# Performance work log

Hardware: AMD Instinct MI355X
Metric: run time of the kernel (lower is better)

The kernel has to match this reference:

```python
import jax, jax.numpy as jnp
import numpy as np

B, IN, H, F, T = 4096, 1024, 1024, 128, 3
LN_EPS = 1e-5


def setup_inputs() -> dict:
    key = jax.random.key(0)
    ks = jax.random.split(key, 12)
    inp = {
        "input_": jax.random.normal(ks[0], (B, IN), jnp.float32),
        "hx": jax.random.normal(ks[1], (B, H), jnp.float32),
        "cx": jax.random.normal(ks[2], (B, H), jnp.float32),
        "topic_w": jax.random.uniform(ks[3], (B, T), jnp.float32),
        # factorized gate weights (init scales per reset_parameters)
        "w_ih_a": jax.random.normal(ks[4], (4 * H, F), jnp.float32) / jnp.sqrt(F),
        "w_ih_b": jnp.full((F, T), 0.1 / T, jnp.float32),
        "w_ih_c": jax.random.normal(ks[5], (F, IN), jnp.float32) / jnp.sqrt(IN),
        "w_hh_a": 0.1 * jax.random.normal(ks[6], (4 * H, F), jnp.float32),
        "w_hh_b": jnp.full((F, T), 0.1 / T, jnp.float32),
        "w_hh_c": 0.1 * jax.random.normal(ks[7], (F, H), jnp.float32),
        # theta transforms: weight=0, bias=1 per reset_parameters
        "th_ih_w": jnp.zeros((T, T), jnp.float32),
        "th_ih_b": jnp.ones((T,), jnp.float32),
        "th_hh_w": jnp.zeros((T, T), jnp.float32),
        "th_hh_b": jnp.ones((T,), jnp.float32),
        # layernorm params
        "ln_i_w": jnp.ones((4 * H,), jnp.float32),
        "ln_i_b": jnp.zeros((4 * H,), jnp.float32),
        "ln_h_w": jnp.ones((4 * H,), jnp.float32),
        "ln_h_b": jnp.zeros((4 * H,), jnp.float32),
        "ln_c_w": jnp.ones((H,), jnp.float32),
        "ln_c_b": jnp.zeros((H,), jnp.float32),
    }
    return inp


def _ln(x, w, b):
    mu = x.mean(-1, keepdims=True)
    var = ((x - mu) ** 2).mean(-1, keepdims=True)
    return (x - mu) * jax.lax.rsqrt(var + LN_EPS) * w + b


def reference(input_, hx, cx, topic_w,
              w_ih_a, w_ih_b, w_ih_c, w_hh_a, w_hh_b, w_hh_c,
              th_ih_w, th_ih_b, th_hh_w, th_hh_b,
              ln_i_w, ln_i_b, ln_h_w, ln_h_b, ln_c_w, ln_c_b):
    # factorized input gates: ((x @ C^T) * (theta(topic) @ B^T)) @ A^T
    scale_i = (topic_w @ th_ih_w.T + th_ih_b) @ w_ih_b.T            # [B, F]
    igates = ((input_ @ w_ih_c.T) * scale_i) @ w_ih_a.T             # [B, 4H]
    scale_h = (topic_w @ th_hh_w.T + th_hh_b) @ w_hh_b.T            # [B, F]
    hgates = ((hx @ w_hh_c.T) * scale_h) @ w_hh_a.T                 # [B, 4H]

    gates = _ln(igates, ln_i_w, ln_i_b) + _ln(hgates, ln_h_w, ln_h_b)
    i, f, g, o = jnp.split(gates, 4, axis=1)
    i = jax.nn.sigmoid(i)
    f = jax.nn.sigmoid(f)
    g = jnp.tanh(g)  # dropout p=0 -> identity
    o = jax.nn.sigmoid(o)
    cy = _ln(f * cx + i * g, ln_c_w, ln_c_b)
    hy = o * jnp.tanh(cy)
    return hy, cy
```

## Files before the change

kernel.cpp:

```cpp
#include <hip/hip_runtime.h>

typedef unsigned short ushort_t;
typedef __attribute__((ext_vector_type(8))) short bf8_t;
typedef __attribute__((ext_vector_type(4))) float f4_t;

#define B_   4096
#define IN_  1024
#define H_   1024
#define F_   128
#define EPS_ 1e-5f

#define NG1   1024
#define NPREP 256
#define NGRAM 128

__device__ __forceinline__ float us2f(unsigned short s) {
  union { unsigned int u; float f; } v;
  v.u = ((unsigned int)s) << 16;
  return v.f;
}
__device__ __forceinline__ unsigned short f2us(float f) {
  union { float f; unsigned int u; } v;
  v.f = f;
  unsigned int r = (v.u + 0x7fffu + ((v.u >> 16) & 1u)) >> 16;
  return (unsigned short)r;
}
__device__ __forceinline__ float sigf(float x) { return 1.0f / (1.0f + __expf(-x)); }
__device__ __forceinline__ float tanh_f(float x) { return 1.0f - 2.0f / (1.0f + __expf(2.0f * x)); }

__device__ __forceinline__ int detect_fp32(const void* disc) {
  return ((const unsigned int*)disc)[0] == 0x3F800000u;
}
__device__ __forceinline__ float ldf(const void* p, int i, int fp32) {
  return fp32 ? ((const float*)p)[i] : us2f(((const ushort_t*)p)[i]);
}
__device__ __forceinline__ void ld8(const void* p, int idx, float* o, int fp32) {
  if (fp32) {
    const float4* q = (const float4*)((const float*)p + idx);
    float4 v0 = q[0], v1 = q[1];
    o[0]=v0.x; o[1]=v0.y; o[2]=v0.z; o[3]=v0.w;
    o[4]=v1.x; o[5]=v1.y; o[6]=v1.z; o[7]=v1.w;
  } else {
    uint4 v = *(const uint4*)((const ushort_t*)p + idx);
    const ushort_t* pv = (const ushort_t*)&v;
    #pragma unroll
    for (int i = 0; i < 8; i++) o[i] = us2f(pv[i]);
  }
}
__device__ __forceinline__ bf8_t cvt8p(const float* f) {
  union { bf8_t v; unsigned int u[4]; } r;
  const unsigned int* ui = (const unsigned int*)f;
  #pragma unroll
  for (int i = 0; i < 4; i++) {
    unsigned int lo = ui[2 * i] + 0x8000u;
    unsigned int hi = ui[2 * i + 1] + 0x8000u;
    r.u[i] = __builtin_amdgcn_perm(hi, lo, 0x07060302u);
  }
  return r.v;
}

__global__ __launch_bounds__(256, 8) void k_stageA(
    const void* __restrict__ X0, const void* __restrict__ X1,
    const void* __restrict__ Wc0, const void* __restrict__ Wc1,
    const void* __restrict__ Ai, const void* __restrict__ Ah,
    const void* __restrict__ lnwi, const void* __restrict__ lnwh,
    ushort_t* __restrict__ wb,
    float* __restrict__ cm_i, float* __restrict__ cm_h,
    float* __restrict__ g_i, float* __restrict__ g_h,
    float* __restrict__ C0, float* __restrict__ C1)
{
  __shared__ __align__(16) char lds_raw[16384];
  int bid = blockIdx.x, tid = threadIdx.x;
  int fp32 = detect_fp32(lnwi);

  if (bid < NG1) {
    int rb = bid >> 2, mat = (bid >> 1) & 1, kh = bid & 1;
    const void* X = mat ? X1 : X0;
    const void* W = mat ? Wc1 : Wc0;
    float* C = mat ? C1 : C0;
    int lane = tid & 63, w = tid >> 6;
    int quad = lane >> 4, lcol = lane & 15;
    int brow0 = rb * 16, k0 = kh * 512;

    #pragma unroll
    for (int p = 0; p < 4; p++) {
      int fl = p * 2048 + tid * 8;
      int r = fl >> 9, cidx = fl & 511;
      float t8[8];
      ld8(X, (brow0 + r) * IN_ + k0 + cidx, t8, fp32);
      bf8_t v = cvt8p(t8);
      int byte = (r * 1024 + cidx * 2) ^ ((r & 7) << 4);
      *(bf8_t*)(lds_raw + byte) = v;
    }
    __syncthreads();

    f4_t acc[2];
    acc[0] = (f4_t){0.f, 0.f, 0.f, 0.f};
    acc[1] = (f4_t){0.f, 0.f, 0.f, 0.f};

    int wrow = w * 32 + lcol;
    int quad8 = quad * 8;
    int afbase = lcol * 1024 + quad * 16;
    int afxor = (lcol & 7) << 4;

#define AF_(kc) (*(const bf8_t*)(lds_raw + ((afbase + (kc) * 64) ^ afxor)))
#define LOADW_(buf, kc) { \
      ld8(W, (wrow)      * IN_ + k0 + (kc) * 32 + quad8, buf[0], fp32); \
      ld8(W, (wrow + 16) * IN_ + k0 + (kc) * 32 + quad8, buf[1], fp32); }
#define STEPK_(buf, kc) { \
      bf8_t af_ = AF_(kc); \
      acc[0] = __builtin_amdgcn_mfma_f32_16x16x32_bf16(af_, cvt8p(buf[0]), acc[0], 0, 0, 0); \
      acc[1] = __builtin_amdgcn_mfma_f32_16x16x32_bf16(af_, cvt8p(buf[1]), acc[1], 0, 0, 0); }

    float pb0[2][8], pb1[2][8];
    LOADW_(pb0, 0);
    LOADW_(pb1, 1);
    #pragma unroll
    for (int kc = 0; kc < 16; kc += 2) {
      STEPK_(pb0, kc);
      if (kc + 2 < 16) LOADW_(pb0, kc + 2);
      STEPK_(pb1, kc + 1);
      if (kc + 3 < 16) LOADW_(pb1, kc + 3);
    }
#undef AF_
#undef LOADW_
#undef STEPK_

    #pragma unroll
    for (int t = 0; t < 2; t++) {
      int f = (w * 2 + t) * 16 + lcol;
      #pragma unroll
      for (int reg = 0; reg < 4; reg++)
        atomicAdd(&C[(brow0 + quad * 4 + reg) * F_ + f], acc[t][reg]);
    }
  } else if (bid < NG1 + NPREP) {
    int t = bid - NG1;
    #pragma unroll
    for (int i = 0; i < 16; i++) {
      int e = i * 256 + tid;
      int c = e >> 9, l = (e >> 3) & 63, j = e & 7;
      int k = c * 32 + ((l >> 4) << 3) + j;
      int n = t * 16 + (l & 15);
      float v;
      if (k < 128) v = ldf(Ai, n * F_ + k, fp32) * ldf(lnwi, n, fp32);
      else         v = ldf(Ah, n * F_ + (k - 128), fp32) * ldf(lnwh, n, fp32);
      wb[(size_t)t * 4096 + e] = f2us(v);
    }
    const void* A = (tid < 128) ? Ai : Ah;
    float* cm = (tid < 128) ? cm_i : cm_h;
    int f = tid & 127;
    float s = 0.f;
    #pragma unroll
    for (int i = 0; i < 16; i++) s += ldf(A, (t * 16 + i) * F_ + f, fp32);
    atomicAdd(&cm[f], s);
  } else {
    int g = bid - (NG1 + NPREP);
    int fblk = g & 3, mat = (g >> 2) & 1, z = g >> 3;
    const void* A = mat ? Ah : Ai;
    float* G = mat ? g_h : g_i;
    float (*As)[128] = (float(*)[128])lds_raw;
    int f1_0 = fblk * 32;
    int tf2 = tid & 31, tf1 = tid >> 5;
    float acc[4][4] = {};
    int nbase = z * 256;
    for (int n0 = nbase; n0 < nbase + 256; n0 += 32) {
      #pragma unroll
      for (int j = 0; j < 2; j++) {
        int idx = tid + 256 * j;
        int nn = idx >> 4, f8 = (idx & 15) * 8;
        float t[8];
        ld8(A, (n0 + nn) * F_ + f8, t, fp32);
        #pragma unroll
        for (int i = 0; i < 8; i++) As[nn][f8 + i] = t[i];
      }
      __syncthreads();
      #pragma unroll 4
      for (int nn = 0; nn < 32; nn++) {
        float4 a1 = *(const float4*)&As[nn][f1_0 + 4 * tf1];
        float4 a2 = *(const float4*)&As[nn][4 * tf2];
        const float* x1 = (const float*)&a1;
        const float* x2 = (const float*)&a2;
        #pragma unroll
        for (int i = 0; i < 4; i++)
          #pragma unroll
          for (int j = 0; j < 4; j++) acc[i][j] += x1[i] * x2[j];
      }
      __syncthreads();
    }
    #pragma unroll
    for (int i = 0; i < 4; i++)
      #pragma unroll
      for (int j = 0; j < 4; j++)
        atomicAdd(&G[(f1_0 + 4 * tf1 + i) * F_ + 4 * tf2 + j], acc[i][j]);
  }
}

__global__ __launch_bounds__(1024) void k_fused2(
    const float* __restrict__ C0g, const float* __restrict__ C1g,
    const float* __restrict__ g_i, const float* __restrict__ g_h,
    const float* __restrict__ cm_i, const float* __restrict__ cm_h,
    const void* __restrict__ topic,
    const void* __restrict__ thw0, const void* __restrict__ thw1,
    const void* __restrict__ thb0, const void* __restrict__ thb1,
    const void* __restrict__ wsb0, const void* __restrict__ wsb1,
    const ushort_t* __restrict__ wb,
    const void* __restrict__ lniw, const void* __restrict__ lnib,
    const void* __restrict__ lnhw, const void* __restrict__ lnhb,
    const void* __restrict__ lncw, const void* __restrict__ lncb,
    const void* __restrict__ cx, float* __restrict__ out)
{
  __shared__ float Cs[2][16][132];
  __shared__ __align__(16) ushort_t xs[4096];
  __shared__ float buf[16][1028];
  __shared__ float obuf[16][1028];
  __shared__ float p1part[2][4][16];
  __shared__ float p2s[2][16];
  __shared__ float rs2_s[2][16];
  __shared__ float mrs_s[2][16];
  __shared__ float wpart[16][16][2];
  __shared__ float mu_s[16], rs_s[16];

  int tid = threadIdx.x;
  int lane = tid & 63, w = tid >> 6;
  int quad = lane >> 4, lcol = lane & 15;
  int b0 = blockIdx.x * 16;
  int fp32 = detect_fp32(lniw);

  {
    int mat = tid >> 9, rem = tid & 511;
    int row = rem >> 5, f0 = (rem & 31) * 4;
    const float* C = mat ? C1g : C0g;
    const void* thw = mat ? thw1 : thw0;
    const void* thb = mat ? thb1 : thb0;
    const void* wbp = mat ? wsb1 : wsb0;
    float tp0 = ldf(topic, (b0 + row) * 3 + 0, fp32);
    float tp1 = ldf(topic, (b0 + row) * 3 + 1, fp32);
    float tp2 = ldf(topic, (b0 + row) * 3 + 2, fp32);
    float tv[3];
    #pragma unroll
    for (int t = 0; t < 3; t++)
      tv[t] = ldf(thb, t, fp32) + tp0 * ldf(thw, t * 3 + 0, fp32)
            + tp1 * ldf(thw, t * 3 + 1, fp32) + tp2 * ldf(thw, t * 3 + 2, fp32);
    float4 v = *(const float4*)&C[(size_t)(b0 + row) * F_ + f0];
    const float* vp = (const float*)&v;
    #pragma unroll
    for (int j = 0; j < 4; j++) {
      int f = f0 + j;
      float sc = tv[0] * ldf(wbp, f * 3 + 0, fp32)
               + tv[1] * ldf(wbp, f * 3 + 1, fp32)
               + tv[2] * ldf(wbp, f * 3 + 2, fp32);
      Cs[mat][row][f] = vp[j] * sc;
    }
  }
  __syncthreads();

  if (w < 8) {
    int w2 = w & 3, smat = w >> 2;
    const float* G  = smat ? g_h : g_i;
    const float* cm = smat ? cm_h : cm_i;
    bf8_t af[4];
    float p2p = 0.f;
    #pragma unroll
    for (int kc = 0; kc < 4; kc++) {
      int kb = kc * 32 + quad * 8;
      float a[8];
      #pragma unroll
      for (int j = 0; j < 8; j++) a[j] = Cs[smat][lcol][kb + j];
      af[kc] = cvt8p(a);
      if (w2 == 0) {
        #pragma unroll
        for (int j = 0; j < 8; j++) p2p += a[j] * cm[kb + j];
      }
    }
    float p1p[4] = {0.f, 0.f, 0.f, 0.f};
    #pragma unroll
    for (int t = 0; t < 2; t++) {
      int colf = (w2 * 2 + t) * 16 + lcol;
      f4_t acc = {0.f, 0.f, 0.f, 0.f};
      #pragma unroll
      for (int kc = 0; kc < 4; kc++) {
        const float4* qg = (const float4*)(G + colf * F_ + kc * 32 + quad * 8);
        float4 w0 = qg[0], w1 = qg[1];
        float bt[8] = {w0.x, w0.y, w0.z, w0.w, w1.x, w1.y, w1.z, w1.w};
        acc = __builtin_amdgcn_mfma_f32_16x16x32_bf16(af[kc], cvt8p(bt), acc, 0, 0, 0);
      }
      #pragma unroll
      for (int reg = 0; reg < 4; reg++)
        p1p[reg] += acc[reg] * Cs[smat][quad * 4 + reg][colf];
    }
    #pragma unroll
    for (int d = 1; d < 16; d <<= 1)
      #pragma unroll
      for (int reg = 0; reg < 4; reg++)
        p1p[reg] += __shfl_xor(p1p[reg], d, 64);
    if (lcol == 0) {
      #pragma unroll
      for (int reg = 0; reg < 4; reg++)
        p1part[smat][w2][quad * 4 + reg] = p1p[reg];
    }
    if (w2 == 0) {
      p2p += __shfl_xor(p2p, 16, 64);
      p2p += __shfl_xor(p2p, 32, 64);
      if (quad == 0) p2s[smat][lcol] = p2p;
    }
  }
  __syncthreads();
  if (tid < 32) {
    int m = tid >> 4, r = tid & 15;
    float p1 = p1part[m][0][r] + p1part[m][1][r] + p1part[m][2][r] + p1part[m][3][r];
    float E2 = p1 * (1.0f / 4096.0f);
    float mu = p2s[m][r] * (1.0f / 4096.0f);
    float rs = rsqrtf(E2 - mu * mu + EPS_);
    rs2_s[m][r] = rs;
    mrs_s[m][r] = mu * rs;
  }
  __syncthreads();

  if (tid < 512) {
    int m = tid >> 8, tt = tid & 255;
    int f = tt & 127, half = tt >> 7;
    int k = m * 128 + f;
    int c = k >> 5, lq = (k >> 3) & 3, j = k & 7;
    #pragma unroll
    for (int i = 0; i < 8; i++) {
      int r2 = half * 8 + i;
      int lfrag = r2 | (lq << 4);
      xs[c * 512 + lfrag * 8 + j] = f2us(Cs[m][r2][f] * rs2_s[m][r2]);
    }
  }
  __syncthreads();

  float mi[4], mh[4];
  #pragma unroll
  for (int reg = 0; reg < 4; reg++) {
    mi[reg] = mrs_s[0][quad * 4 + reg];
    mh[reg] = mrs_s[1][quad * 4 + reg];
  }

  float s1[4] = {0.f, 0.f, 0.f, 0.f}, s2[4] = {0.f, 0.f, 0.f, 0.f};

  #pragma unroll
  for (int q = 0; q < 4; q++) {
    int cg = w * 4 + q;
    int col = cg * 16 + lcol;
    float cxv[4];
    #pragma unroll
    for (int reg = 0; reg < 4; reg++)
      cxv[reg] = ldf(cx, (size_t)(b0 + quad * 4 + reg) * H_ + col, fp32);

    f4_t accg[4];
    #pragma unroll
    for (int g = 0; g < 4; g++) accg[g] = (f4_t){0.f, 0.f, 0.f, 0.f};
    #pragma unroll
    for (int c = 0; c < 8; c++) {
      bf8_t af = *(const bf8_t*)&xs[c * 512 + lane * 8];
      #pragma unroll
      for (int g = 0; g < 4; g++) {
        bf8_t bf = *(const bf8_t*)(wb + (size_t)(g * 64 + cg) * 4096 + c * 512 + lane * 8);
        accg[g] = __builtin_amdgcn_mfma_f32_16x16x32_bf16(af, bf, accg[g], 0, 0, 0);
      }
    }
    float liw0 = ldf(lniw, 0 * H_ + col, fp32), lib0 = ldf(lnib, 0 * H_ + col, fp32);
    float lhw0 = ldf(lnhw, 0 * H_ + col, fp32), lhb0 = ldf(lnhb, 0 * H_ + col, fp32);
    float liw1 = ldf(lniw, 1 * H_ + col, fp32), lib1 = ldf(lnib, 1 * H_ + col, fp32);
    float lhw1 = ldf(lnhw, 1 * H_ + col, fp32), lhb1 = ldf(lnhb, 1 * H_ + col, fp32);
    float liw2 = ldf(lniw, 2 * H_ + col, fp32), lib2 = ldf(lnib, 2 * H_ + col, fp32);
    float lhw2 = ldf(lnhw, 2 * H_ + col, fp32), lhb2 = ldf(lnhb, 2 * H_ + col, fp32);
    float liw3 = ldf(lniw, 3 * H_ + col, fp32), lib3 = ldf(lnib, 3 * H_ + col, fp32);
    float lhw3 = ldf(lnhw, 3 * H_ + col, fp32), lhb3 = ldf(lnhb, 3 * H_ + col, fp32);
    #pragma unroll
    for (int reg = 0; reg < 4; reg++) {
      int m = quad * 4 + reg;
      float gi = accg[0][reg] + lib0 + lhb0 - mi[reg] * liw0 - mh[reg] * lhw0;
      float gf = accg[1][reg] + lib1 + lhb1 - mi[reg] * liw1 - mh[reg] * lhw1;
      float gg = accg[2][reg] + lib2 + lhb2 - mi[reg] * liw2 - mh[reg] * lhw2;
      float go = accg[3][reg] + lib3 + lhb3 - mi[reg] * liw3 - mh[reg] * lhw3;
      float iv = sigf(gi), fv = sigf(gf), gv = tanh_f(gg), ov = sigf(go);
      float cval = fv * cxv[reg] + iv * gv;
      buf[m][col] = cval;
      obuf[m][col] = ov;
      s1[reg] += cval;
      s2[reg] += cval * cval;
    }
  }

  #pragma unroll
  for (int d = 1; d < 16; d <<= 1) {
    #pragma unroll
    for (int reg = 0; reg < 4; reg++) {
      s1[reg] += __shfl_xor(s1[reg], d, 64);
      s2[reg] += __shfl_xor(s2[reg], d, 64);
    }
  }
  if (lcol == 0) {
    #pragma unroll
    for (int reg = 0; reg < 4; reg++) {
      wpart[w][quad * 4 + reg][0] = s1[reg];
      wpart[w][quad * 4 + reg][1] = s2[reg];
    }
  }
  __syncthreads();
  if (tid < 16) {
    float t1 = 0.f, t2 = 0.f;
    #pragma unroll
    for (int ww = 0; ww < 16; ww++) { t1 += wpart[ww][tid][0]; t2 += wpart[ww][tid][1]; }
    float mu = t1 * (1.0f / 1024.0f);
    float var = t2 * (1.0f / 1024.0f) - mu * mu;
    mu_s[tid] = mu;
    rs_s[tid] = rsqrtf(var + EPS_);
  }
  __syncthreads();

  #pragma unroll
  for (int q = 0; q < 4; q++) {
    int col = (w * 4 + q) * 16 + lcol;
    float lw = ldf(lncw, col, fp32), lb = ldf(lncb, col, fp32);
    #pragma unroll
    for (int reg = 0; reg < 4; reg++) {
      int m = quad * 4 + reg;
      float cyv = (buf[m][col] - mu_s[m]) * rs_s[m] * lw + lb;
      out[(size_t)B_ * H_ + (size_t)(b0 + m) * H_ + col] = cyv;
      out[(size_t)(b0 + m) * H_ + col] = obuf[m][col] * tanh_f(cyv);
    }
  }
}

extern "C" void kernel_launch(void* const* d_in, const int* in_sizes, int n_in,
                              void* d_out, int out_size, void* d_ws, size_t ws_size,
                              hipStream_t stream) {
  const void* input_  = d_in[0];
  const void* hx      = d_in[1];
  const void* cx      = d_in[2];
  const void* topic   = d_in[3];
  const void* w_ih_a  = d_in[4];
  const void* w_ih_b  = d_in[5];
  const void* w_ih_c  = d_in[6];
  const void* w_hh_a  = d_in[7];
  const void* w_hh_b  = d_in[8];
  const void* w_hh_c  = d_in[9];
  const void* th_ih_w = d_in[10];
  const void* th_ih_b = d_in[11];
  const void* th_hh_w = d_in[12];
  const void* th_hh_b = d_in[13];
  const void* ln_i_w  = d_in[14];
  const void* ln_i_b  = d_in[15];
  const void* ln_h_w  = d_in[16];
  const void* ln_h_b  = d_in[17];
  const void* ln_c_w  = d_in[18];
  const void* ln_c_b  = d_in[19];

  float* w = (float*)d_ws;
  float* c1    = w;
  float* c2    = c1 + B_ * F_;
  float* g_i   = c2 + B_ * F_;
  float* g_h   = g_i + F_ * F_;
  float* cm_i  = g_h + F_ * F_;
  float* cm_h  = cm_i + F_;
  ushort_t* wbf = (ushort_t*)(cm_h + F_);

  hipMemsetAsync(c1, 0, (size_t)(2 * B_ * F_ + 2 * F_ * F_ + 2 * F_) * sizeof(float), stream);

  k_stageA<<<dim3(NG1 + NPREP + NGRAM), dim3(256), 0, stream>>>(
      input_, hx, w_ih_c, w_hh_c,
      w_ih_a, w_hh_a, ln_i_w, ln_h_w,
      wbf, cm_i, cm_h, g_i, g_h, c1, c2);
  k_fused2<<<dim3(256), dim3(1024), 0, stream>>>(
      c1, c2, g_i, g_h, cm_i, cm_h,
      topic, th_ih_w, th_hh_w, th_ih_b, th_hh_b, w_ih_b, w_hh_b,
      wbf, ln_i_w, ln_i_b, ln_h_w, ln_h_b, ln_c_w, ln_c_b, cx, (float*)d_out);
}
```

Baseline: 218.4 us.

## Stage X and W tiles via global_load_lds over full K, drop split-K atomics

```diff
diff --git a/kernel.cpp b/kernel.cpp
--- a/kernel.cpp
+++ b/kernel.cpp
@@ -10,9 +10,15 @@
 #define F_   128
 #define EPS_ 1e-5f
 
-#define NG1   1024
+#define NG1   512
 #define NPREP 256
 #define NGRAM 128
+
+#define KC_   64
+#define NCH_  16
+#define XSZ_  4096
+#define WSZ_  32768
+#define LDSZ_ 36864
 
 __device__ __forceinline__ float us2f(unsigned short s) {
   union { unsigned int u; float f; } v;
@@ -59,7 +65,13 @@
   return r.v;
 }
 
-__global__ __launch_bounds__(256, 8) void k_stageA(
+__device__ __forceinline__ void gl_lds16(const void* g, void* l) {
+  __builtin_amdgcn_global_load_lds(
+      (const __attribute__((address_space(1))) unsigned int*)g,
+      (__attribute__((address_space(3))) unsigned int*)l, 16, 0, 0);
+}
+
+__global__ __launch_bounds__(256, 4) void k_stageA(
     const void* __restrict__ X0, const void* __restrict__ X1,
     const void* __restrict__ Wc0, const void* __restrict__ Wc1,
     const void* __restrict__ Ai, const void* __restrict__ Ah,
@@ -69,69 +81,71 @@
     float* __restrict__ g_i, float* __restrict__ g_h,
     float* __restrict__ C0, float* __restrict__ C1)
 {
-  __shared__ __align__(16) char lds_raw[16384];
+  __shared__ __align__(16) char lds_raw[LDSZ_];
   int bid = blockIdx.x, tid = threadIdx.x;
   int fp32 = detect_fp32(lnwi);
 
   if (bid < NG1) {
-    int rb = bid >> 2, mat = (bid >> 1) & 1, kh = bid & 1;
-    const void* X = mat ? X1 : X0;
-    const void* W = mat ? Wc1 : Wc0;
+    int rb = bid >> 1, mat = bid & 1;
+    const char* Xc = (const char*)(mat ? X1 : X0);
+    const char* Wc = (const char*)(mat ? Wc1 : Wc0);
     float* C = mat ? C1 : C0;
     int lane = tid & 63, w = tid >> 6;
     int quad = lane >> 4, lcol = lane & 15;
-    int brow0 = rb * 16, k0 = kh * 512;
-
-    #pragma unroll
-    for (int p = 0; p < 4; p++) {
-      int fl = p * 2048 + tid * 8;
-      int r = fl >> 9, cidx = fl & 511;
-      float t8[8];
-      ld8(X, (brow0 + r) * IN_ + k0 + cidx, t8, fp32);
-      bf8_t v = cvt8p(t8);
-      int byte = (r * 1024 + cidx * 2) ^ ((r & 7) << 4);
-      *(bf8_t*)(lds_raw + byte) = v;
-    }
-    __syncthreads();
+    int brow0 = rb * 16;
+
+    const char* srcp[9];
+    #pragma unroll
+    for (int j = 0; j < 9; j++) {
+      int flat = (w * 9 + j) * 1024 + (lane << 4);
+      if (flat < XSZ_) {
+        int r = flat >> 8, inb = flat & 255;
+        srcp[j] = Xc + (size_t)(brow0 + r) * 4096 + (inb ^ ((r & 7) << 5));
+      } else {
+        int fw = flat - XSZ_;
+        int r = fw >> 8, inb = fw & 255;
+        srcp[j] = Wc + (size_t)r * 4096 + (inb ^ ((r & 7) << 5));
+      }
+    }
 
     f4_t acc[2];
     acc[0] = (f4_t){0.f, 0.f, 0.f, 0.f};
     acc[1] = (f4_t){0.f, 0.f, 0.f, 0.f};
 
-    int wrow = w * 32 + lcol;
-    int quad8 = quad * 8;
-    int afbase = lcol * 1024 + quad * 16;
-    int afxor = (lcol & 7) << 4;
-
-#define AF_(kc) (*(const bf8_t*)(lds_raw + ((afbase + (kc) * 64) ^ afxor)))
-#define LOADW_(buf, kc) { \
-      ld8(W, (wrow)      * IN_ + k0 + (kc) * 32 + quad8, buf[0], fp32); \
-      ld8(W, (wrow + 16) * IN_ + k0 + (kc) * 32 + quad8, buf[1], fp32); }
-#define STEPK_(buf, kc) { \
-      bf8_t af_ = AF_(kc); \
-      acc[0] = __builtin_amdgcn_mfma_f32_16x16x32_bf16(af_, cvt8p(buf[0]), acc[0], 0, 0, 0); \
-      acc[1] = __builtin_amdgcn_mfma_f32_16x16x32_bf16(af_, cvt8p(buf[1]), acc[1], 0, 0, 0); }
-
-    float pb0[2][8], pb1[2][8];
-    LOADW_(pb0, 0);
-    LOADW_(pb1, 1);
-    #pragma unroll
-    for (int kc = 0; kc < 16; kc += 2) {
-      STEPK_(pb0, kc);
-      if (kc + 2 < 16) LOADW_(pb0, kc + 2);
-      STEPK_(pb1, kc + 1);
-      if (kc + 3 < 16) LOADW_(pb1, kc + 3);
-    }
-#undef AF_
-#undef LOADW_
-#undef STEPK_
+    for (int kc0 = 0; kc0 < NCH_; kc0++) {
+      int koff = kc0 * 256;
+      #pragma unroll
+      for (int j = 0; j < 9; j++)
+        gl_lds16(srcp[j] + koff, lds_raw + (w * 9 + j) * 1024);
+      __syncthreads();
+
+      #pragma unroll
+      for (int kc = 0; kc < 2; kc++) {
+        int kb = kc * 128 + quad * 32;
+        int abyte = lcol * 256 + (kb ^ ((lcol & 7) << 5));
+        float4 a0 = *(const float4*)(lds_raw + abyte);
+        float4 a1 = *(const float4*)(lds_raw + abyte + 16);
+        float a8[8] = {a0.x, a0.y, a0.z, a0.w, a1.x, a1.y, a1.z, a1.w};
+        bf8_t af = cvt8p(a8);
+        #pragma unroll
+        for (int t = 0; t < 2; t++) {
+          int f = w * 32 + t * 16 + lcol;
+          int wbyte = XSZ_ + f * 256 + (kb ^ ((f & 7) << 5));
+          float4 b0 = *(const float4*)(lds_raw + wbyte);
+          float4 b1 = *(const float4*)(lds_raw + wbyte + 16);
+          float b8[8] = {b0.x, b0.y, b0.z, b0.w, b1.x, b1.y, b1.z, b1.w};
+          acc[t] = __builtin_amdgcn_mfma_f32_16x16x32_bf16(af, cvt8p(b8), acc[t], 0, 0, 0);
+        }
+      }
+      __syncthreads();
+    }
 
     #pragma unroll
     for (int t = 0; t < 2; t++) {
-      int f = (w * 2 + t) * 16 + lcol;
+      int f = w * 32 + t * 16 + lcol;
       #pragma unroll
       for (int reg = 0; reg < 4; reg++)
-        atomicAdd(&C[(brow0 + quad * 4 + reg) * F_ + f], acc[t][reg]);
+        C[(brow0 + quad * 4 + reg) * F_ + f] = acc[t][reg];
     }
   } else if (bid < NG1 + NPREP) {
     int t = bid - NG1;
@@ -458,7 +472,7 @@
   float* cm_h  = cm_i + F_;
   ushort_t* wbf = (ushort_t*)(cm_h + F_);
 
-  hipMemsetAsync(c1, 0, (size_t)(2 * B_ * F_ + 2 * F_ * F_ + 2 * F_) * sizeof(float), stream);
+  hipMemsetAsync(g_i, 0, (size_t)(2 * F_ * F_ + 2 * F_) * sizeof(float), stream);
 
   k_stageA<<<dim3(NG1 + NPREP + NGRAM), dim3(256), 0, stream>>>(
       input_, hx, w_ih_c, w_hh_c,
```

Result: faster. 199.7 us (-8.6%).
